# Kernel tuning notes

Hardware: AMD Instinct MI355X
Metric: run time of the kernel (lower is better)

The kernel has to match this reference:

```python
import jax, jax.numpy as jnp
import numpy as np

B, T, H, NH = 4, 4096, 768, 12
D = H          # attention inner dim (expand_ratio = 1)
I = 4 * H      # MLP intermediate size


def rms_norm(x, eps=1e-6):
    return x * jax.lax.rsqrt(jnp.mean(x * x, axis=-1, keepdims=True) + eps)


def layer_norm(x, eps=1e-6):
    mu = jnp.mean(x, axis=-1, keepdims=True)
    var = jnp.mean((x - mu) ** 2, axis=-1, keepdims=True)
    return (x - mu) * jax.lax.rsqrt(var + eps)


def act_quant(x):
    # per-token int8 absmax quantization (BitNet b1.58)
    scale = 127.0 / jnp.maximum(jnp.max(jnp.abs(x), axis=-1, keepdims=True), 1e-5)
    return jnp.clip(jnp.round(x * scale), -128, 127) / scale


def weight_quant(w):
    # per-tensor ternary quantization
    scale = 1.0 / jnp.maximum(jnp.mean(jnp.abs(w)), 1e-5)
    return jnp.clip(jnp.round(w * scale), -1, 1) / scale


def bit_linear(x, w, b=None):
    xn = rms_norm(x)
    xq = xn + jax.lax.stop_gradient(act_quant(xn) - xn)  # STE
    wq = w + jax.lax.stop_gradient(weight_quant(w) - w)  # STE
    y = jnp.einsum('...k,nk->...n', xq, wq)
    return y if b is None else y + b


def setup_inputs() -> dict:
    key = jax.random.key(0)
    ks = jax.random.split(key, 12)
    s = 0.02
    return dict(
        x=jax.random.normal(ks[0], (B, T, H), jnp.float32),
        c=jax.random.normal(ks[1], (B, H), jnp.float32),
        w_emb=jax.random.normal(ks[2], (2 * H, H), jnp.float32) * s,
        b_emb=jnp.zeros((2 * H,), jnp.float32),
        w_i=jax.random.normal(ks[3], (D, H), jnp.float32) * s,
        w_f=jax.random.normal(ks[4], (D, H), jnp.float32) * s,
        w_g=jax.random.normal(ks[5], (D, H), jnp.float32) * s,
        w_gn=jnp.ones((D,), jnp.float32),
        w_o=jax.random.normal(ks[6], (H, D), jnp.float32) * s,
        w_gate=jax.random.normal(ks[7], (2 * I, H), jnp.float32) * s,
        w_down=jax.random.normal(ks[8], (H, I), jnp.float32) * s,
        w_proj=jax.random.normal(ks[9], (H, 2 * H), jnp.float32) * s,
        b_proj=jnp.zeros((H,), jnp.float32),
    )


def reference(x, c, w_emb, b_emb, w_i, w_f, w_g, w_gn, w_o,
              w_gate, w_down, w_proj, b_proj):
    # --- AdaLayerNormZeroSingle ---
    emb = jnp.einsum('bk,nk->bn', jax.nn.silu(c), w_emb) + b_emb   # [B, 2H]
    scale, gate = jnp.split(emb, 2, axis=-1)                        # [B, H] each
    nx = layer_norm(x) * (1.0 + scale[:, None, :])                  # [B, T, H]

    # --- HGRNBitAttention: gated elementwise linear recurrence ---
    i = bit_linear(nx, w_i)                                         # [B, T, D]
    f = jax.nn.sigmoid(bit_linear(nx, w_f))                         # forget gate
    i = jax.nn.silu(i) * (1.0 - f)                                  # input gate

    def step(h, inp):
        it, ft = inp
        h = ft * h + it
        return h, h

    h0 = jnp.zeros((x.shape[0], i.shape[-1]), x.dtype)
    _, o = jax.lax.scan(step, h0, (jnp.swapaxes(i, 0, 1), jnp.swapaxes(f, 0, 1)))
    o = jnp.swapaxes(o, 0, 1)                                       # [B, T, D]

    g = bit_linear(nx, w_g)
    o = rms_norm(o) * w_gn * jax.nn.silu(g)                         # RMSNorm swish gate
    attn_out = bit_linear(o, w_o)                                   # [B, T, H]

    # --- HGRNBitMLP ---
    y = bit_linear(nx, w_gate)                                      # [B, T, 2I]
    g_m, y = jnp.split(y, 2, axis=-1)
    mlp_out = bit_linear(jax.nn.silu(g_m) * y, w_down)              # [B, T, H]

    # --- concat, project, gate, residual ---
    hs = jnp.concatenate([attn_out, mlp_out], axis=-1)              # [B, T, 2H]
    hs = gate[:, None, :] * bit_linear(hs, w_proj, b_proj)
    return x + hs
```

## Files before the change

kernel.cpp:

```cpp
#include <hip/hip_runtime.h>
#include <hip/hip_bf16.h>
#include <stdint.h>

#define HD 768
#define BB 4
#define TT 4096
#define NT (BB*TT)
#define IM 3072
#define NCH 128
#define CHL (TT/NCH)
#define MCH 4
#define MCT (NT/MCH)

typedef int v4i __attribute__((ext_vector_type(4)));
typedef __hip_bfloat16 bf16;
typedef unsigned int uint32;

__device__ __forceinline__ float wave_sum(float v){
#pragma unroll
  for (int o=32;o;o>>=1) v += __shfl_down(v,o);
  return v;
}
__device__ __forceinline__ float wave_sum_x(float v){
#pragma unroll
  for (int o=32;o;o>>=1) v += __shfl_xor(v,o);
  return v;
}
__device__ __forceinline__ float wave_max_x(float v){
#pragma unroll
  for (int o=32;o;o>>=1) v = fmaxf(v,__shfl_xor(v,o));
  return v;
}
__device__ __forceinline__ float block_sum(float v, float* lds){
  const int nw = blockDim.x >> 6;
  v = wave_sum(v);
  if ((threadIdx.x&63)==0) lds[threadIdx.x>>6] = v;
  __syncthreads();
  float r = lds[0];
  for (int i=1;i<nw;++i) r += lds[i];
  __syncthreads();
  return r;
}
__device__ __forceinline__ float sigmoidf_(float x){ return __builtin_amdgcn_rcpf(1.f + __expf(-x)); }
__device__ __forceinline__ float siluf_(float x){ return x * __builtin_amdgcn_rcpf(1.f + __expf(-x)); }
__device__ __forceinline__ float b2f(bf16 v){ return __bfloat162float(v); }
__device__ __forceinline__ bf16  f2b(float v){ return __float2bfloat16(v); }
__device__ __forceinline__ float bfb2f(uint32 u16){ uint32 v = u16<<16; return __builtin_bit_cast(float, v); }
__device__ __forceinline__ uint16_t packq2(float q0, float q1){
  int a = (int)q0, b = (int)q1;
  return (uint16_t)((a&0xff) | ((b&0xff)<<8));
}
__device__ __forceinline__ uint32 packq4(float a, float b, float c, float d){
  return (uint32)((int)a&0xff) | (((uint32)((int)b&0xff))<<8) |
         (((uint32)((int)c&0xff))<<16) | (((uint32)((int)d&0xff))<<24);
}
__device__ __forceinline__ uint32 pack2bf(float a, float b){
  uint32 ua = __builtin_bit_cast(uint16_t, f2b(a));
  uint32 ub = __builtin_bit_cast(uint16_t, f2b(b));
  return ua | (ub<<16);
}
__device__ __forceinline__ float clampq(float v){ return fminf(fmaxf(v,-128.f),127.f); }
__device__ __forceinline__ void gl_lds16(const int8_t* g, void* l){
  __builtin_amdgcn_global_load_lds((const __attribute__((address_space(1))) void*)g,
                                   (__attribute__((address_space(3))) void*)l, 16, 0, 0);
}

struct WArgs { const float* p[7]; int n[7]; size_t off[7]; };

#define WC1 589824
#define WC2 1179648
#define WC3 1769472
#define WC4 2359296
#define WC5 7077888
#define WC6 9437184
#define WCT 10616832

__global__ __launch_bounds__(256) void absum_part_all(WArgs wa, float* __restrict__ part){
  __shared__ float lds[8];
  const int seg = blockIdx.y;
  const int n4 = wa.n[seg] >> 2;
  const float4* w = (const float4*)wa.p[seg];
  float s = 0.f;
  for (int i = blockIdx.x*256 + threadIdx.x; i < n4; i += gridDim.x*256){
    float4 v = w[i];
    s += (fabsf(v.x)+fabsf(v.y)) + (fabsf(v.z)+fabsf(v.w));
  }
  s = block_sum(s, lds);
  if (threadIdx.x==0) part[seg*64 + blockIdx.x] = s;
}
__global__ __launch_bounds__(512) void absum_final_all(const float* __restrict__ part, WArgs wa,
                                                       float* __restrict__ wscv, float* __restrict__ wrec){
  int seg = threadIdx.x >> 6, lane = threadIdx.x & 63;
  float v = (seg < 7) ? part[seg*64 + lane] : 0.f;
  v = wave_sum(v);
  if (seg < 7 && lane == 0){
    float m = fmaxf(v / (float)wa.n[seg], 1e-5f);
    wscv[seg] = m; wrec[seg] = 1.f/m;
  }
}
__global__ __launch_bounds__(256) void wquant_all(WArgs wa, const float* __restrict__ wrec,
                                                  int8_t* __restrict__ q){
  const int seg = blockIdx.y;
  const int n4 = wa.n[seg] >> 2;
  const float4* p = (const float4*)wa.p[seg];
  uint32* qo = (uint32*)(q + wa.off[seg]);
  const float rc = wrec[seg];
  for (int i = blockIdx.x*256 + threadIdx.x; i < n4; i += gridDim.x*256){
    float4 v = p[i];
    int a  = (int)fminf(fmaxf(rintf(v.x*rc),-1.f),1.f);
    int b  = (int)fminf(fmaxf(rintf(v.y*rc),-1.f),1.f);
    int cc = (int)fminf(fmaxf(rintf(v.z*rc),-1.f),1.f);
    int d  = (int)fminf(fmaxf(rintf(v.w*rc),-1.f),1.f);
    qo[i] = (uint32)(a&0xff) | ((uint32)(b&0xff)<<8) | ((uint32)(cc&0xff)<<16) | ((uint32)(d&0xff)<<24);
  }
}

__global__ __launch_bounds__(256) void ada_emb(const float* __restrict__ c, const float* __restrict__ w_emb,
                                               const float* __restrict__ b_emb,
                                               float* __restrict__ scaleA, float* __restrict__ gateA){
  int o = blockIdx.x*4 + (threadIdx.x>>6);
  int lane = threadIdx.x & 63;
  int b = o / 1536, n = o % 1536;
  const float* cr = c + b*HD;
  const float* wr = w_emb + (size_t)n*HD;
  float s = 0.f;
  for (int k=lane; k<HD; k+=64){
    float cv = cr[k];
    s += siluf_(cv)*wr[k];
  }
  s = wave_sum(s);
  if (lane==0){
    s += b_emb[n];
    if (n < HD) scaleA[b*HD+n] = s;
    else        gateA[b*HD+(n-HD)] = s;
  }
}

__global__ __launch_bounds__(256) void ln_quant(const float* __restrict__ x, const float* __restrict__ scaleA,
                                                int8_t* __restrict__ xq, float* __restrict__ rsx){
  const int tok  = blockIdx.x*4 + (threadIdx.x>>6);
  const int lane = threadIdx.x & 63;
  const int b = tok >> 12;
  const float4* xr = (const float4*)(x + (size_t)tok*HD);
  const float4* sr = (const float4*)(scaleA + (size_t)b*HD);
  float4 v[3];
  float s1 = 0.f, s2 = 0.f;
#pragma unroll
  for (int j=0;j<3;++j){
    v[j] = xr[lane + j*64];
    s1 += (v[j].x+v[j].y)+(v[j].z+v[j].w);
    s2 += (v[j].x*v[j].x+v[j].y*v[j].y)+(v[j].z*v[j].z+v[j].w*v[j].w);
  }
  s1 = wave_sum_x(s1); s2 = wave_sum_x(s2);
  const float mu  = s1 * (1.f/768.f);
  const float var = fmaxf(s2 * (1.f/768.f) - mu*mu, 0.f);
  const float r1  = rsqrtf(var + 1e-6f);
  float sv[12]; float ms = 0.f, amr = 0.f;
#pragma unroll
  for (int j=0;j<3;++j){
    float4 sc = sr[lane + j*64];
    float a0 = (v[j].x-mu)*r1*(1.f+sc.x);
    float a1 = (v[j].y-mu)*r1*(1.f+sc.y);
    float a2 = (v[j].z-mu)*r1*(1.f+sc.z);
    float a3 = (v[j].w-mu)*r1*(1.f+sc.w);
    sv[4*j]=a0; sv[4*j+1]=a1; sv[4*j+2]=a2; sv[4*j+3]=a3;
    ms += (a0*a0+a1*a1)+(a2*a2+a3*a3);
    amr = fmaxf(amr, fmaxf(fmaxf(fabsf(a0),fabsf(a1)),fmaxf(fabsf(a2),fabsf(a3))));
  }
  ms = wave_sum_x(ms); amr = wave_max_x(amr);
  const float r2 = rsqrtf(ms*(1.f/768.f) + 1e-6f);
  const float am = fmaxf(amr*r2, 1e-5f);
  const float sx = 127.f/am;
  uint32* qo = (uint32*)(xq + (size_t)tok*HD);
#pragma unroll
  for (int j=0;j<3;++j){
    qo[lane + j*64] = packq4(clampq(rintf(sv[4*j]*r2*sx)),   clampq(rintf(sv[4*j+1]*r2*sx)),
                             clampq(rintf(sv[4*j+2]*r2*sx)), clampq(rintf(sv[4*j+3]*r2*sx)));
  }
  if (lane==0) rsx[tok] = am*(1.f/127.f);
}

template<int C>
__global__ __launch_bounds__(256) void rms_quant_w(const uint32* __restrict__ zin, int8_t* __restrict__ q,
                                                   float* __restrict__ rs){
  const int tok  = blockIdx.x*4 + (threadIdx.x>>6);
  const int lane = threadIdx.x & 63;
  const uint32* zp = zin + (size_t)tok*C*64;
  uint32 u[C]; float ss = 0.f, amr = 0.f;
#pragma unroll
  for (int j=0;j<C;++j){
    u[j] = zp[lane + j*64];
    float a = bfb2f(u[j] & 0xffff), b = bfb2f(u[j] >> 16);
    ss += a*a + b*b;
    amr = fmaxf(amr, fmaxf(fabsf(a),fabsf(b)));
  }
  ss = wave_sum_x(ss); amr = wave_max_x(amr);
  const float r = rsqrtf(ss*(1.f/(float)(C*128)) + 1e-6f);
  const float am = fmaxf(amr*r, 1e-5f);
  const float sx = 127.f/am;
  uint16_t* qo = (uint16_t*)(q + (size_t)tok*C*128);
#pragma unroll
  for (int j=0;j<C;++j){
    float a = bfb2f(u[j] & 0xffff), b = bfb2f(u[j] >> 16);
    qo[lane + j*64] = packq2(clampq(rintf(a*r*sx)), clampq(rintf(b*r*sx)));
  }
  if (lane==0) rs[tok] = am*(1.f/127.f);
}

__global__ __launch_bounds__(256) void rms_quant_cat(const uint32* __restrict__ pa, const uint32* __restrict__ pb,
                                                     int8_t* __restrict__ q, float* __restrict__ rs){
  const int tok  = blockIdx.x*4 + (threadIdx.x>>6);
  const int lane = threadIdx.x & 63;
  const uint32* ap = pa + (size_t)tok*(HD/2);
  const uint32* bp = pb + (size_t)tok*(HD/2);
  uint32 u[12]; float ss = 0.f, amr = 0.f;
#pragma unroll
  for (int j=0;j<6;++j){
    u[j] = ap[lane + j*64];
    float a = bfb2f(u[j] & 0xffff), b = bfb2f(u[j] >> 16);
    ss += a*a + b*b;
    amr = fmaxf(amr, fmaxf(fabsf(a),fabsf(b)));
  }
#pragma unroll
  for (int j=0;j<6;++j){
    u[6+j] = bp[lane + j*64];
    float a = bfb2f(u[6+j] & 0xffff), b = bfb2f(u[6+j] >> 16);
    ss += a*a + b*b;
    amr = fmaxf(amr, fmaxf(fabsf(a),fabsf(b)));
  }
  ss = wave_sum_x(ss); amr = wave_max_x(amr);
  const float r = rsqrtf(ss*(1.f/1536.f) + 1e-6f);
  const float am = fmaxf(amr*r, 1e-5f);
  const float sx = 127.f/am;
  uint16_t* qo = (uint16_t*)(q + (size_t)tok*(2*HD));
#pragma unroll
  for (int j=0;j<6;++j){
    float a = bfb2f(u[j] & 0xffff), b = bfb2f(u[j] >> 16);
    qo[lane + j*64] = packq2(clampq(rintf(a*r*sx)), clampq(rintf(b*r*sx)));
  }
#pragma unroll
  for (int j=0;j<6;++j){
    float a = bfb2f(u[6+j] & 0xffff), b = bfb2f(u[6+j] >> 16);
    qo[384 + lane + j*64] = packq2(clampq(rintf(a*r*sx)), clampq(rintf(b*r*sx)));
  }
  if (lane==0) rs[tok] = am*(1.f/127.f);
}

__global__ __launch_bounds__(256) void gate_norm_quant(const uint32* __restrict__ o, const uint32* __restrict__ gs,
                                                       const float* __restrict__ w_gn,
                                                       int8_t* __restrict__ oq, float* __restrict__ rso){
  const int tok  = blockIdx.x*4 + (threadIdx.x>>6);
  const int lane = threadIdx.x & 63;
  const uint32* op = o  + (size_t)tok*(HD/2);
  const uint32* gp = gs + (size_t)tok*(HD/2);
  const float2* wg = (const float2*)w_gn;
  uint32 u[6]; float ms = 0.f;
#pragma unroll
  for (int j=0;j<6;++j){
    u[j] = op[lane + j*64];
    float a = bfb2f(u[j] & 0xffff), b = bfb2f(u[j] >> 16);
    ms += a*a + b*b;
  }
  ms = wave_sum_x(ms);
  const float rn = rsqrtf(ms*(1.f/768.f) + 1e-6f);
  float uu[12]; float ms2 = 0.f, amr = 0.f;
#pragma unroll
  for (int j=0;j<6;++j){
    uint32 g = gp[lane + j*64];
    float2 w = wg[lane + j*64];
    float a = bfb2f(u[j] & 0xffff)*rn*w.x*bfb2f(g & 0xffff);
    float b = bfb2f(u[j] >> 16)  *rn*w.y*bfb2f(g >> 16);
    uu[2*j]=a; uu[2*j+1]=b;
    ms2 += a*a + b*b;
    amr = fmaxf(amr, fmaxf(fabsf(a),fabsf(b)));
  }
  ms2 = wave_sum_x(ms2); amr = wave_max_x(amr);
  const float r2 = rsqrtf(ms2*(1.f/768.f) + 1e-6f);
  const float am = fmaxf(amr*r2, 1e-5f);
  const float sx = 127.f/am;
  uint16_t* qo = (uint16_t*)(oq + (size_t)tok*HD);
#pragma unroll
  for (int j=0;j<6;++j){
    qo[lane + j*64] = packq2(clampq(rintf(uu[2*j]*r2*sx)), clampq(rintf(uu[2*j+1]*r2*sx)));
  }
  if (lane==0) rso[tok] = am*(1.f/127.f);
}

__global__ __launch_bounds__(384) void scan_pass1(const uint32* __restrict__ iact, const uint32* __restrict__ fsig,
                                                  float* __restrict__ chF, float* __restrict__ chH){
  const int blk = blockIdx.x;
  const int b = blk >> 7, ch = blk & (NCH-1);
  const int t0 = b*TT + ch*CHL;
  const size_t base = (size_t)t0*(HD/2) + threadIdx.x;
  float F0=1.f,F1=1.f,h0=0.f,h1=0.f;
#pragma unroll 4
  for (int s=0;s<CHL;++s){
    uint32 fu = fsig[base + (size_t)s*(HD/2)];
    uint32 iu = iact[base + (size_t)s*(HD/2)];
    float f0 = bfb2f(fu&0xffff), f1 = bfb2f(fu>>16);
    float a0 = bfb2f(iu&0xffff), a1 = bfb2f(iu>>16);
    h0 = f0*h0 + a0; h1 = f1*h1 + a1;
    F0 *= f0; F1 *= f1;
  }
  size_t cb = (size_t)blk*HD + 2*threadIdx.x;
  *(float2*)(chF + cb) = make_float2(F0,F1);
  *(float2*)(chH + cb) = make_float2(h0,h1);
}
__global__ __launch_bounds__(256) void scan_combine(float* __restrict__ chF, float* __restrict__ chH){
  const int gid = blockIdx.x*256 + threadIdx.x;
  const int b = gid / HD, d = gid % HD;
  float h = 0.f;
#pragma unroll 8
  for (int c=0;c<NCH;++c){
    size_t idx = (size_t)(b*NCH+c)*HD + d;
    float F = chF[idx], Hl = chH[idx];
    chH[idx] = h;
    h = F*h + Hl;
  }
}
__global__ __launch_bounds__(384) void scan_pass2(const uint32* iact, const uint32* __restrict__ fsig,
                                                  const float* __restrict__ chH, uint32* o){
  const int blk = blockIdx.x;
  const int b = blk >> 7, ch = blk & (NCH-1);
  const int t0 = b*TT + ch*CHL;
  const size_t base = (size_t)t0*(HD/2) + threadIdx.x;
  float2 hin = *(const float2*)(chH + (size_t)blk*HD + 2*threadIdx.x);
  float h0 = hin.x, h1 = hin.y;
#pragma unroll 4
  for (int s=0;s<CHL;++s){
    uint32 fu = fsig[base + (size_t)s*(HD/2)];
    uint32 iu = iact[base + (size_t)s*(HD/2)];
    float f0 = bfb2f(fu&0xffff), f1 = bfb2f(fu>>16);
    float a0 = bfb2f(iu&0xffff), a1 = bfb2f(iu>>16);
    h0 = f0*h0 + a0; h1 = f1*h1 + a1;
    uint16_t pa = __builtin_bit_cast(uint16_t, f2b(h0));
    uint16_t pb = __builtin_bit_cast(uint16_t, f2b(h1));
    o[base + (size_t)s*(HD/2)] = (uint32)pa | ((uint32)pb<<16);
  }
}

enum { EPI_IF=0, EPI_SILU=1, EPI_STORE=2, EPI_SWIGLU=3, EPI_PROJ=4 };

template<int EPI, bool DUAL>
__global__ __launch_bounds__(512) void gemm_i8(
    const int8_t* __restrict__ A, const float* __restrict__ rsA,
    const int8_t* __restrict__ B0, const int8_t* __restrict__ B1,
    const float* __restrict__ ws0p, const float* __restrict__ ws1p,
    int K, void* __restrict__ out0v, void* __restrict__ out1v,
    int ldOut, int colOff,
    const float* __restrict__ bias, const float* __restrict__ gateA,
    const float* __restrict__ xres)
{
  __shared__ __align__(16) uint8_t sA [2][16384];
  __shared__ __align__(16) uint8_t sB0[2][8192];
  __shared__ __align__(16) uint8_t sB1[DUAL?2:1][8192];

  const int lane = threadIdx.x & 63;
  const int wv   = threadIdx.x >> 6;
  const int m0 = blockIdx.x*256;
  const int n0 = blockIdx.y*128;
  const int wm = (wv>>1)*64;
  const int wn = (wv&1)*64;
  const int lr = lane & 15;
  const int sl = lane >> 4;

  const int8_t* gA[2]; const int8_t* gB0; const int8_t* gB1;
  int ldsOffA[2], ldsOffB;
#pragma unroll
  for (int j=0;j<2;++j){
    int q = wv*2 + j;
    int r = q*16 + (lane>>2);
    int cg = (lane&3) ^ ((r>>1)&3);
    gA[j] = A + (size_t)(m0+r)*K + cg*16;
    ldsOffA[j] = q*1024;
  }
  {
    int r = wv*16 + (lane>>2);
    int cg = (lane&3) ^ ((r>>1)&3);
    gB0 = B0 + (size_t)(n0+r)*K + cg*16;
    gB1 = DUAL ? (B1 + (size_t)(n0+r)*K + cg*16) : (const int8_t*)0;
    ldsOffB = wv*1024;
  }
  int offA[4], offB[4];
#pragma unroll
  for (int i=0;i<4;++i){
    int Ra = wm + i*16 + lr;
    offA[i] = Ra*64 + ((sl ^ ((Ra>>1)&3))<<4);
    int Rb = wn + i*16 + lr;
    offB[i] = Rb*64 + ((sl ^ ((Rb>>1)&3))<<4);
  }

  v4i acc0[4][4], acc1[4][4];
  const v4i vzero = {0,0,0,0};
#pragma unroll
  for (int i=0;i<4;++i)
#pragma unroll
    for (int j=0;j<4;++j){ acc0[i][j]=vzero; acc1[i][j]=vzero; }

  const int NTI = K >> 6;
#pragma unroll
  for (int j=0;j<2;++j) gl_lds16(gA[j], &sA[0][ldsOffA[j]]);
  gl_lds16(gB0, &sB0[0][ldsOffB]);
  if (DUAL) gl_lds16(gB1, &sB1[0][ldsOffB]);
#pragma unroll
  for (int j=0;j<2;++j) gl_lds16(gA[j]+64, &sA[1][ldsOffA[j]]);
  gl_lds16(gB0+64, &sB0[1][ldsOffB]);
  if (DUAL) gl_lds16(gB1+64, &sB1[1][ldsOffB]);

  int cur = 0;
  for (int t=0; t<NTI; ++t){
    if (t+1 < NTI){
      if constexpr (DUAL) asm volatile("s_waitcnt vmcnt(4)" ::: "memory");
      else                asm volatile("s_waitcnt vmcnt(3)" ::: "memory");
    } else {
      asm volatile("s_waitcnt vmcnt(0)" ::: "memory");
    }
    asm volatile("s_barrier" ::: "memory");

    v4i av[4], b0v[4], b1v[4];
#pragma unroll
    for (int i=0;i<4;++i){
      av[i]  = *(const v4i*)&sA [cur][offA[i]];
      b0v[i] = *(const v4i*)&sB0[cur][offB[i]];
    }
    if constexpr (DUAL){
#pragma unroll
      for (int i=0;i<4;++i) b1v[i] = *(const v4i*)&sB1[cur][offB[i]];
    }
    asm volatile("s_waitcnt lgkmcnt(0)" ::: "memory");
    asm volatile("s_barrier" ::: "memory");

    if (t+2 < NTI){
      const int ko = (t+2)*64;
#pragma unroll
      for (int j=0;j<2;++j) gl_lds16(gA[j]+ko, &sA[cur][ldsOffA[j]]);
      gl_lds16(gB0+ko, &sB0[cur][ldsOffB]);
      if (DUAL) gl_lds16(gB1+ko, &sB1[cur][ldsOffB]);
    }
    __builtin_amdgcn_sched_barrier(0);

    __builtin_amdgcn_s_setprio(1);
#pragma unroll
    for (int mi=0;mi<4;++mi){
#pragma unroll
      for (int ni=0;ni<4;++ni){
        acc0[mi][ni] = __builtin_amdgcn_mfma_i32_16x16x64_i8(b0v[ni], av[mi], acc0[mi][ni], 0,0,0);
        if constexpr (DUAL)
          acc1[mi][ni] = __builtin_amdgcn_mfma_i32_16x16x64_i8(b1v[ni], av[mi], acc1[mi][ni], 0,0,0);
      }
    }
    __builtin_amdgcn_s_setprio(0);
    cur ^= 1;
  }

  const float w0 = *ws0p;
  const float w1 = DUAL ? *ws1p : 0.f;
  const int rb = sl*4;
  const int em0 = m0 + wm, en0 = n0 + wn;
#pragma unroll
  for (int mi=0;mi<4;++mi){
    const int tok = em0 + mi*16 + lr;
    const float rs = rsA[tok];
#pragma unroll
    for (int ni=0;ni<4;++ni){
      const int ch = en0 + ni*16 + rb;
      float y0[4], y1[4];
#pragma unroll
      for (int r=0;r<4;++r){
        y0[r] = (float)acc0[mi][ni][r] * rs * w0;
        if constexpr (DUAL) y1[r] = (float)acc1[mi][ni][r] * rs * w1;
      }
      if constexpr (EPI==EPI_IF){
        float fs[4], io[4];
#pragma unroll
        for (int r=0;r<4;++r){ fs[r] = sigmoidf_(y1[r]); io[r] = siluf_(y0[r])*(1.f-fs[r]); }
        uint2 ui, uf;
        ui.x = pack2bf(io[0],io[1]); ui.y = pack2bf(io[2],io[3]);
        uf.x = pack2bf(fs[0],fs[1]); uf.y = pack2bf(fs[2],fs[3]);
        *(uint2*)((bf16*)out0v + (size_t)tok*ldOut + ch) = ui;
        *(uint2*)((bf16*)out1v + (size_t)tok*ldOut + ch) = uf;
      } else if constexpr (EPI==EPI_SILU){
        uint2 u;
        u.x = pack2bf(siluf_(y0[0]), siluf_(y0[1]));
        u.y = pack2bf(siluf_(y0[2]), siluf_(y0[3]));
        *(uint2*)((bf16*)out0v + (size_t)tok*ldOut + ch) = u;
      } else if constexpr (EPI==EPI_STORE){
        uint2 u;
        u.x = pack2bf(y0[0],y0[1]); u.y = pack2bf(y0[2],y0[3]);
        *(uint2*)((bf16*)out0v + (size_t)tok*ldOut + colOff + ch) = u;
      } else if constexpr (EPI==EPI_SWIGLU){
        uint2 u;
        u.x = pack2bf(siluf_(y0[0])*y1[0], siluf_(y0[1])*y1[1]);
        u.y = pack2bf(siluf_(y0[2])*y1[2], siluf_(y0[3])*y1[3]);
        *(uint2*)((bf16*)out0v + (size_t)tok*ldOut + ch) = u;
      } else {
        const int bidx = tok >> 12;
        float4 b4 = *(const float4*)(bias + ch);
        float4 g4 = *(const float4*)(gateA + bidx*HD + ch);
        float4 x4 = *(const float4*)(xres + (size_t)tok*HD + ch);
        float4 o4;
        o4.x = x4.x + g4.x*(y0[0] + b4.x);
        o4.y = x4.y + g4.y*(y0[1] + b4.y);
        o4.z = x4.z + g4.z*(y0[2] + b4.z);
        o4.w = x4.w + g4.w*(y0[3] + b4.w);
        *(float4*)((float*)out0v + (size_t)tok*HD + ch) = o4;
      }
    }
  }
}

extern "C" void kernel_launch(void* const* d_in, const int* in_sizes, int n_in,
                              void* d_out, int out_size, void* d_ws, size_t ws_size,
                              hipStream_t stream){
  const float* x      = (const float*)d_in[0];
  const float* c      = (const float*)d_in[1];
  const float* w_emb  = (const float*)d_in[2];
  const float* b_emb  = (const float*)d_in[3];
  const float* w_i    = (const float*)d_in[4];
  const float* w_f    = (const float*)d_in[5];
  const float* w_g    = (const float*)d_in[6];
  const float* w_gn   = (const float*)d_in[7];
  const float* w_o    = (const float*)d_in[8];
  const float* w_gate = (const float*)d_in[9];
  const float* w_down = (const float*)d_in[10];
  const float* w_proj = (const float*)d_in[11];
  const float* b_proj = (const float*)d_in[12];
  float* out = (float*)d_out;
  char* ws = (char*)d_ws;

  constexpr size_t SZ_HH   = (size_t)HD*HD;
  constexpr size_t o_wq     = 0;
  constexpr size_t o_wsc    = o_wq + (size_t)WCT;
  constexpr size_t o_wrecip = o_wsc    + 256;
  constexpr size_t o_part   = o_wrecip + 256;
  constexpr size_t o_scaleA = o_part   + 2048;
  constexpr size_t o_gateA  = o_scaleA + (size_t)BB*HD*4;
  constexpr size_t o_rsx    = o_gateA  + (size_t)BB*HD*4;
  constexpr size_t o_rso    = o_rsx    + (size_t)NT*4;
  constexpr size_t o_rsh    = o_rso    + (size_t)NT*4;
  constexpr size_t o_rsm    = o_rsh    + (size_t)NT*4;
  constexpr size_t o_xq     = o_rsm    + (size_t)NT*4;
  constexpr size_t o_END0   = o_xq     + (size_t)NT*HD;

  constexpr size_t o_R1     = o_END0;
  constexpr size_t o_R2     = o_R1     + (size_t)NT*HD*2;
  constexpr size_t o_R3     = o_R2     + (size_t)NT*HD*2;
  constexpr size_t o_chF    = o_R3     + (size_t)NT*HD*2;
  constexpr size_t o_chH    = o_chF    + (size_t)BB*NCH*HD*4;
  constexpr size_t o_R4     = o_chH    + (size_t)BB*NCH*HD*4;
  constexpr size_t NEED_S   = o_R4     + (size_t)NT*HD;

  constexpr size_t o_Z      = o_END0;
  constexpr size_t o_M      = o_Z + (size_t)NT*IM*2;
  constexpr size_t o_chF2   = o_M + (size_t)NT*IM;
  constexpr size_t o_chH2   = o_chF2 + (size_t)BB*NCH*HD*4;
  constexpr size_t NEED_B   = o_chH2 + (size_t)BB*NCH*HD*4;

  if (ws_size < NEED_S) return;
  const bool big = (ws_size >= NEED_B);

  float*  wscv  = (float*)(ws + o_wsc);
  float*  wrec  = (float*)(ws + o_wrecip);
  float*  part  = (float*)(ws + o_part);
  float*  scaleA= (float*)(ws + o_scaleA);
  float*  gateA = (float*)(ws + o_gateA);
  float*  rsx   = (float*)(ws + o_rsx);
  float*  rso   = (float*)(ws + o_rso);
  float*  rsh   = (float*)(ws + o_rsh);
  float*  rsm   = (float*)(ws + o_rsm);
  int8_t* xq    = (int8_t*)(ws + o_xq);
  int8_t* wqall = (int8_t*)(ws + o_wq);
  int8_t* wqp[7] = { wqall, wqall+WC1, wqall+WC2, wqall+WC3, wqall+WC4, wqall+WC5, wqall+WC6 };

  WArgs wa;
  wa.p[0]=w_i; wa.p[1]=w_f; wa.p[2]=w_g; wa.p[3]=w_o; wa.p[4]=w_gate; wa.p[5]=w_down; wa.p[6]=w_proj;
  wa.n[0]=(int)SZ_HH; wa.n[1]=(int)SZ_HH; wa.n[2]=(int)SZ_HH; wa.n[3]=(int)SZ_HH;
  wa.n[4]=2*IM*HD; wa.n[5]=HD*IM; wa.n[6]=HD*2*HD;
  wa.off[0]=0; wa.off[1]=WC1; wa.off[2]=WC2; wa.off[3]=WC3; wa.off[4]=WC4; wa.off[5]=WC5; wa.off[6]=WC6;

  absum_part_all <<<dim3(64,7),  dim3(256), 0, stream>>>(wa, part);
  absum_final_all<<<dim3(1),     dim3(512), 0, stream>>>(part, wa, wscv, wrec);
  wquant_all     <<<dim3(256,7), dim3(256), 0, stream>>>(wa, wrec, wqall);
  ada_emb <<<dim3(1536), dim3(256), 0, stream>>>(c, w_emb, b_emb, scaleA, gateA);
  ln_quant<<<dim3(NT/4), dim3(256), 0, stream>>>(x, scaleA, xq, rsx);

  if (big){
    bf16* zc      = (bf16*)(ws + o_Z);
    bf16* iact    = (bf16*)(ws + o_Z);
    bf16* fsig    = (bf16*)(ws + o_Z + (size_t)NT*HD*2);
    bf16* gsilu   = (bf16*)(ws + o_Z + (size_t)2*NT*HD*2);
    bf16* attn    = gsilu;
    bf16* mlp     = (bf16*)(ws + o_Z + (size_t)3*NT*HD*2);
    int8_t* mq    = (int8_t*)(ws + o_M);
    int8_t* oq    = (int8_t*)(ws + o_M);
    int8_t* hq    = (int8_t*)(ws + o_M + (size_t)NT*HD);
    float* chF    = (float*)(ws + o_chF2);
    float* chH    = (float*)(ws + o_chH2);
    bf16* obuf    = iact;

    gemm_i8<EPI_SWIGLU,true><<<dim3(NT/256,24), dim3(512), 0, stream>>>(
        xq, rsx, wqp[4], wqp[4] + (size_t)IM*HD, wscv+4, wscv+4, HD,
        zc, nullptr, IM, 0, nullptr, nullptr, nullptr);
    rms_quant_w<24><<<dim3(NT/4), dim3(256), 0, stream>>>((const uint32*)zc, mq, rsm);
    gemm_i8<EPI_STORE,false><<<dim3(NT/256,6), dim3(512), 0, stream>>>(
        mq, rsm, wqp[5], nullptr, wscv+5, nullptr, IM, mlp, nullptr, HD, 0, nullptr, nullptr, nullptr);

    gemm_i8<EPI_IF,true><<<dim3(NT/256,6), dim3(512), 0, stream>>>(
        xq, rsx, wqp[0], wqp[1], wscv+0, wscv+1, HD, iact, fsig, HD, 0, nullptr, nullptr, nullptr);
    gemm_i8<EPI_SILU,false><<<dim3(NT/256,6), dim3(512), 0, stream>>>(
        xq, rsx, wqp[2], nullptr, wscv+2, nullptr, HD, gsilu, nullptr, HD, 0, nullptr, nullptr, nullptr);
    scan_pass1 <<<dim3(BB*NCH), dim3(384), 0, stream>>>((const uint32*)iact, (const uint32*)fsig, chF, chH);
    scan_combine<<<dim3(12),    dim3(256), 0, stream>>>(chF, chH);
    scan_pass2 <<<dim3(BB*NCH), dim3(384), 0, stream>>>((const uint32*)iact, (const uint32*)fsig, chH, (uint32*)obuf);
    gate_norm_quant<<<dim3(NT/4), dim3(256), 0, stream>>>((const uint32*)obuf, (const uint32*)gsilu, w_gn, oq, rso);
    gemm_i8<EPI_STORE,false><<<dim3(NT/256,6), dim3(512), 0, stream>>>(
        oq, rso, wqp[3], nullptr, wscv+3, nullptr, HD, attn, nullptr, HD, 0, nullptr, nullptr, nullptr);

    rms_quant_cat<<<dim3(NT/4), dim3(256), 0, stream>>>((const uint32*)attn, (const uint32*)mlp, hq, rsh);
    gemm_i8<EPI_PROJ,false><<<dim3(NT/256,6), dim3(512), 0, stream>>>(
        hq, rsh, wqp[6], nullptr, wscv+6, nullptr, 2*HD, out, nullptr, HD, 0, b_proj, gateA, x);
  } else {
    bf16*   iact  = (bf16*)(ws + o_R1);
    bf16*   fsig  = (bf16*)(ws + o_R2);
    bf16*   gsilu = (bf16*)(ws + o_R3);
    bf16*   obuf  = iact;
    bf16*   hs    = (bf16*)(ws + o_R1);
    bf16*   zc    = (bf16*)(ws + o_R3);
    int8_t* hq    = (int8_t*)(ws + o_R3);
    float*  chF   = (float*)(ws + o_chF);
    float*  chH   = (float*)(ws + o_chH);
    int8_t* oq    = (int8_t*)(ws + o_R4);
    int8_t* mq    = (int8_t*)(ws + o_R4);

    gemm_i8<EPI_IF,true><<<dim3(NT/256,6), dim3(512), 0, stream>>>(
        xq, rsx, wqp[0], wqp[1], wscv+0, wscv+1, HD, iact, fsig, HD, 0, nullptr, nullptr, nullptr);
    gemm_i8<EPI_SILU,false><<<dim3(NT/256,6), dim3(512), 0, stream>>>(
        xq, rsx, wqp[2], nullptr, wscv+2, nullptr, HD, gsilu, nullptr, HD, 0, nullptr, nullptr, nullptr);
    scan_pass1 <<<dim3(BB*NCH), dim3(384), 0, stream>>>((const uint32*)iact, (const uint32*)fsig, chF, chH);
    scan_combine<<<dim3(12),    dim3(256), 0, stream>>>(chF, chH);
    scan_pass2 <<<dim3(BB*NCH), dim3(384), 0, stream>>>((const uint32*)iact, (const uint32*)fsig, chH, (uint32*)obuf);
    gate_norm_quant<<<dim3(NT/4), dim3(256), 0, stream>>>((const uint32*)obuf, (const uint32*)gsilu, w_gn, oq, rso);
    gemm_i8<EPI_STORE,false><<<dim3(NT/256,6), dim3(512), 0, stream>>>(
        oq, rso, wqp[3], nullptr, wscv+3, nullptr, HD, hs, nullptr, 2*HD, 0, nullptr, nullptr, nullptr);
    for (int cc=0; cc<MCH; ++cc){
      const size_t r0 = (size_t)cc*MCT;
      gemm_i8<EPI_SWIGLU,true><<<dim3(MCT/256,24), dim3(512), 0, stream>>>(
          xq + r0*HD, rsx + r0, wqp[4], wqp[4] + (size_t)IM*HD, wscv+4, wscv+4, HD,
          zc, nullptr, IM, 0, nullptr, nullptr, nullptr);
      rms_quant_w<24><<<dim3(MCT/4), dim3(256), 0, stream>>>((const uint32*)zc, mq, rsm);
      gemm_i8<EPI_STORE,false><<<dim3(MCT/256,6), dim3(512), 0, stream>>>(
          mq, rsm, wqp[5], nullptr, wscv+5, nullptr, IM,
          hs + r0*2*HD, nullptr, 2*HD, HD, nullptr, nullptr, nullptr);
    }
    rms_quant_w<12><<<dim3(NT/4), dim3(256), 0, stream>>>((const uint32*)hs, hq, rsh);
    gemm_i8<EPI_PROJ,false><<<dim3(NT/256,6), dim3(512), 0, stream>>>(
        hq, rsh, wqp[6], nullptr, wscv+6, nullptr, 2*HD, out, nullptr, HD, 0, b_proj, gateA, x);
  }

  (void)in_sizes; (void)n_in; (void)out_size;
}
```

Baseline: 445.7 us.

## Switch int8 GEMM to 32x32x32 MFMA with triple-buffered LDS pipeline

Replaces the 16x16x64 int8 MFMA tiling with 32x32x32 MFMA instructions, so each wave computes 2x2 tiles of 32x32 with 16-wide accumulators. This reduces LDS fragment reads per MFMA. The shared-memory ring grows from two to three stages, so the next tile's loads are issued before compute and only one barrier runs per iteration instead of two. LDS use rises (about 96KB for the dual variant), which may reduce occupancy. The epilogue is remapped to the 32x32 output layout.

New measurement: 504.1 us. 1.13x slower.

```diff
diff --git a/kernel.cpp b/kernel.cpp
--- a/kernel.cpp
+++ b/kernel.cpp
@@ -12,7 +12,8 @@
 #define MCH 4
 #define MCT (NT/MCH)
 
-typedef int v4i __attribute__((ext_vector_type(4)));
+typedef int v4i  __attribute__((ext_vector_type(4)));
+typedef int v16i __attribute__((ext_vector_type(16)));
 typedef __hip_bfloat16 bf16;
 typedef unsigned int uint32;
 
@@ -351,9 +352,9 @@
     const float* __restrict__ bias, const float* __restrict__ gateA,
     const float* __restrict__ xres)
 {
-  __shared__ __align__(16) uint8_t sA [2][16384];
-  __shared__ __align__(16) uint8_t sB0[2][8192];
-  __shared__ __align__(16) uint8_t sB1[DUAL?2:1][8192];
+  __shared__ __align__(16) uint8_t sA [3][16384];
+  __shared__ __align__(16) uint8_t sB0[3][8192];
+  __shared__ __align__(16) uint8_t sB1[DUAL?3:1][8192];
 
   const int lane = threadIdx.x & 63;
   const int wv   = threadIdx.x >> 6;
@@ -361,8 +362,8 @@
   const int n0 = blockIdx.y*128;
   const int wm = (wv>>1)*64;
   const int wn = (wv&1)*64;
-  const int lr = lane & 15;
-  const int sl = lane >> 4;
+  const int tokl = lane & 31;
+  const int hi   = lane >> 5;
 
   const int8_t* gA[2]; const int8_t* gB0; const int8_t* gB1;
   int ldsOffA[2], ldsOffB;
@@ -381,129 +382,156 @@
     gB1 = DUAL ? (B1 + (size_t)(n0+r)*K + cg*16) : (const int8_t*)0;
     ldsOffB = wv*1024;
   }
-  int offA[4], offB[4];
-#pragma unroll
-  for (int i=0;i<4;++i){
-    int Ra = wm + i*16 + lr;
-    offA[i] = Ra*64 + ((sl ^ ((Ra>>1)&3))<<4);
-    int Rb = wn + i*16 + lr;
-    offB[i] = Rb*64 + ((sl ^ ((Rb>>1)&3))<<4);
-  }
-
-  v4i acc0[4][4], acc1[4][4];
-  const v4i vzero = {0,0,0,0};
-#pragma unroll
-  for (int i=0;i<4;++i)
-#pragma unroll
-    for (int j=0;j<4;++j){ acc0[i][j]=vzero; acc1[i][j]=vzero; }
+  int offA[2][2], offB[2][2];
+#pragma unroll
+  for (int mi=0;mi<2;++mi)
+#pragma unroll
+    for (int ks=0;ks<2;++ks){
+      int Ra = wm + mi*32 + tokl;
+      offA[mi][ks] = Ra*64 + (((ks*2+hi) ^ ((Ra>>1)&3))<<4);
+    }
+#pragma unroll
+  for (int ni=0;ni<2;++ni)
+#pragma unroll
+    for (int ks=0;ks<2;++ks){
+      int Rb = wn + ni*32 + tokl;
+      offB[ni][ks] = Rb*64 + (((ks*2+hi) ^ ((Rb>>1)&3))<<4);
+    }
+
+  v16i acc0[2][2], acc1[2][2];
+  const v16i vzero = {0,0,0,0,0,0,0,0,0,0,0,0,0,0,0,0};
+#pragma unroll
+  for (int i=0;i<2;++i)
+#pragma unroll
+    for (int j=0;j<2;++j){ acc0[i][j]=vzero; acc1[i][j]=vzero; }
 
   const int NTI = K >> 6;
-#pragma unroll
-  for (int j=0;j<2;++j) gl_lds16(gA[j], &sA[0][ldsOffA[j]]);
-  gl_lds16(gB0, &sB0[0][ldsOffB]);
-  if (DUAL) gl_lds16(gB1, &sB1[0][ldsOffB]);
-#pragma unroll
-  for (int j=0;j<2;++j) gl_lds16(gA[j]+64, &sA[1][ldsOffA[j]]);
-  gl_lds16(gB0+64, &sB0[1][ldsOffB]);
-  if (DUAL) gl_lds16(gB1+64, &sB1[1][ldsOffB]);
-
-  int cur = 0;
+
+#define STAGE(KO, BUF) do { \
+    _Pragma("unroll") \
+    for (int j_=0;j_<2;++j_) gl_lds16(gA[j_]+(KO), &sA[BUF][ldsOffA[j_]]); \
+    gl_lds16(gB0+(KO), &sB0[BUF][ldsOffB]); \
+    if constexpr (DUAL) gl_lds16(gB1+(KO), &sB1[BUF][ldsOffB]); \
+  } while(0)
+
+#define WAIT_VM_LD() do { \
+    if constexpr (DUAL) asm volatile("s_waitcnt vmcnt(4)" ::: "memory"); \
+    else                asm volatile("s_waitcnt vmcnt(3)" ::: "memory"); \
+  } while(0)
+
+  STAGE(0, 0);
+  STAGE(64, 1);
+  WAIT_VM_LD();
+  asm volatile("s_barrier" ::: "memory");
+
+  int bc = 0, bn = 1, bs = 2;
   for (int t=0; t<NTI; ++t){
+    if (t+2 < NTI) STAGE((t+2)*64, bs);
+
+    v4i av[2][2], b0v[2][2], b1v[2][2];
+#pragma unroll
+    for (int mi=0;mi<2;++mi)
+#pragma unroll
+      for (int ks=0;ks<2;++ks)
+        av[mi][ks] = *(const v4i*)&sA[bc][offA[mi][ks]];
+#pragma unroll
+    for (int ni=0;ni<2;++ni)
+#pragma unroll
+      for (int ks=0;ks<2;++ks)
+        b0v[ni][ks] = *(const v4i*)&sB0[bc][offB[ni][ks]];
+    if constexpr (DUAL){
+#pragma unroll
+      for (int ni=0;ni<2;++ni)
+#pragma unroll
+        for (int ks=0;ks<2;++ks)
+          b1v[ni][ks] = *(const v4i*)&sB1[bc][offB[ni][ks]];
+    }
+
+    __builtin_amdgcn_s_setprio(1);
+#pragma unroll
+    for (int mi=0;mi<2;++mi)
+#pragma unroll
+      for (int ni=0;ni<2;++ni){
+        acc0[mi][ni] = __builtin_amdgcn_mfma_i32_32x32x32_i8(b0v[ni][0], av[mi][0], acc0[mi][ni], 0,0,0);
+        if constexpr (DUAL)
+          acc1[mi][ni] = __builtin_amdgcn_mfma_i32_32x32x32_i8(b1v[ni][0], av[mi][0], acc1[mi][ni], 0,0,0);
+      }
+#pragma unroll
+    for (int mi=0;mi<2;++mi)
+#pragma unroll
+      for (int ni=0;ni<2;++ni){
+        acc0[mi][ni] = __builtin_amdgcn_mfma_i32_32x32x32_i8(b0v[ni][1], av[mi][1], acc0[mi][ni], 0,0,0);
+        if constexpr (DUAL)
+          acc1[mi][ni] = __builtin_amdgcn_mfma_i32_32x32x32_i8(b1v[ni][1], av[mi][1], acc1[mi][ni], 0,0,0);
+      }
+    __builtin_amdgcn_s_setprio(0);
+
+    { int tmp = bc; bc = bn; bn = bs; bs = tmp; }
+
     if (t+1 < NTI){
-      if constexpr (DUAL) asm volatile("s_waitcnt vmcnt(4)" ::: "memory");
-      else                asm volatile("s_waitcnt vmcnt(3)" ::: "memory");
-    } else {
-      asm volatile("s_waitcnt vmcnt(0)" ::: "memory");
+      asm volatile("s_waitcnt lgkmcnt(0)" ::: "memory");
+      if (t+2 < NTI) WAIT_VM_LD();
+      else asm volatile("s_waitcnt vmcnt(0)" ::: "memory");
+      asm volatile("s_barrier" ::: "memory");
     }
-    asm volatile("s_barrier" ::: "memory");
-
-    v4i av[4], b0v[4], b1v[4];
-#pragma unroll
-    for (int i=0;i<4;++i){
-      av[i]  = *(const v4i*)&sA [cur][offA[i]];
-      b0v[i] = *(const v4i*)&sB0[cur][offB[i]];
-    }
-    if constexpr (DUAL){
-#pragma unroll
-      for (int i=0;i<4;++i) b1v[i] = *(const v4i*)&sB1[cur][offB[i]];
-    }
-    asm volatile("s_waitcnt lgkmcnt(0)" ::: "memory");
-    asm volatile("s_barrier" ::: "memory");
-
-    if (t+2 < NTI){
-      const int ko = (t+2)*64;
-#pragma unroll
-      for (int j=0;j<2;++j) gl_lds16(gA[j]+ko, &sA[cur][ldsOffA[j]]);
-      gl_lds16(gB0+ko, &sB0[cur][ldsOffB]);
-      if (DUAL) gl_lds16(gB1+ko, &sB1[cur][ldsOffB]);
-    }
-    __builtin_amdgcn_sched_barrier(0);
-
-    __builtin_amdgcn_s_setprio(1);
-#pragma unroll
-    for (int mi=0;mi<4;++mi){
-#pragma unroll
-      for (int ni=0;ni<4;++ni){
-        acc0[mi][ni] = __builtin_amdgcn_mfma_i32_16x16x64_i8(b0v[ni], av[mi], acc0[mi][ni], 0,0,0);
-        if constexpr (DUAL)
-          acc1[mi][ni] = __builtin_amdgcn_mfma_i32_16x16x64_i8(b1v[ni], av[mi], acc1[mi][ni], 0,0,0);
-      }
-    }
-    __builtin_amdgcn_s_setprio(0);
-    cur ^= 1;
-  }
+  }
+
+#undef STAGE
+#undef WAIT_VM_LD
 
   const float w0 = *ws0p;
   const float w1 = DUAL ? *ws1p : 0.f;
-  const int rb = sl*4;
   const int em0 = m0 + wm, en0 = n0 + wn;
 #pragma unroll
-  for (int mi=0;mi<4;++mi){
-    const int tok = em0 + mi*16 + lr;
+  for (int mi=0;mi<2;++mi){
+    const int tok = em0 + mi*32 + tokl;
     const float rs = rsA[tok];
 #pragma unroll
-    for (int ni=0;ni<4;++ni){
-      const int ch = en0 + ni*16 + rb;
-      float y0[4], y1[4];
-#pragma unroll
-      for (int r=0;r<4;++r){
-        y0[r] = (float)acc0[mi][ni][r] * rs * w0;
-        if constexpr (DUAL) y1[r] = (float)acc1[mi][ni][r] * rs * w1;
-      }
-      if constexpr (EPI==EPI_IF){
-        float fs[4], io[4];
-#pragma unroll
-        for (int r=0;r<4;++r){ fs[r] = sigmoidf_(y1[r]); io[r] = siluf_(y0[r])*(1.f-fs[r]); }
-        uint2 ui, uf;
-        ui.x = pack2bf(io[0],io[1]); ui.y = pack2bf(io[2],io[3]);
-        uf.x = pack2bf(fs[0],fs[1]); uf.y = pack2bf(fs[2],fs[3]);
-        *(uint2*)((bf16*)out0v + (size_t)tok*ldOut + ch) = ui;
-        *(uint2*)((bf16*)out1v + (size_t)tok*ldOut + ch) = uf;
-      } else if constexpr (EPI==EPI_SILU){
-        uint2 u;
-        u.x = pack2bf(siluf_(y0[0]), siluf_(y0[1]));
-        u.y = pack2bf(siluf_(y0[2]), siluf_(y0[3]));
-        *(uint2*)((bf16*)out0v + (size_t)tok*ldOut + ch) = u;
-      } else if constexpr (EPI==EPI_STORE){
-        uint2 u;
-        u.x = pack2bf(y0[0],y0[1]); u.y = pack2bf(y0[2],y0[3]);
-        *(uint2*)((bf16*)out0v + (size_t)tok*ldOut + colOff + ch) = u;
-      } else if constexpr (EPI==EPI_SWIGLU){
-        uint2 u;
-        u.x = pack2bf(siluf_(y0[0])*y1[0], siluf_(y0[1])*y1[1]);
-        u.y = pack2bf(siluf_(y0[2])*y1[2], siluf_(y0[3])*y1[3]);
-        *(uint2*)((bf16*)out0v + (size_t)tok*ldOut + ch) = u;
-      } else {
-        const int bidx = tok >> 12;
-        float4 b4 = *(const float4*)(bias + ch);
-        float4 g4 = *(const float4*)(gateA + bidx*HD + ch);
-        float4 x4 = *(const float4*)(xres + (size_t)tok*HD + ch);
-        float4 o4;
-        o4.x = x4.x + g4.x*(y0[0] + b4.x);
-        o4.y = x4.y + g4.y*(y0[1] + b4.y);
-        o4.z = x4.z + g4.z*(y0[2] + b4.z);
-        o4.w = x4.w + g4.w*(y0[3] + b4.w);
-        *(float4*)((float*)out0v + (size_t)tok*HD + ch) = o4;
+    for (int ni=0;ni<2;++ni){
+#pragma unroll
+      for (int q=0;q<4;++q){
+        const int ch = en0 + ni*32 + q*8 + hi*4;
+        float y0[4], y1[4];
+#pragma unroll
+        for (int r=0;r<4;++r){
+          y0[r] = (float)acc0[mi][ni][q*4+r] * rs * w0;
+          if constexpr (DUAL) y1[r] = (float)acc1[mi][ni][q*4+r] * rs * w1;
+        }
+        if constexpr (EPI==EPI_IF){
+          float fs[4], io[4];
+#pragma unroll
+          for (int r=0;r<4;++r){ fs[r] = sigmoidf_(y1[r]); io[r] = siluf_(y0[r])*(1.f-fs[r]); }
+          uint2 ui, uf;
+          ui.x = pack2bf(io[0],io[1]); ui.y = pack2bf(io[2],io[3]);
+          uf.x = pack2bf(fs[0],fs[1]); uf.y = pack2bf(fs[2],fs[3]);
+          *(uint2*)((bf16*)out0v + (size_t)tok*ldOut + ch) = ui;
+          *(uint2*)((bf16*)out1v + (size_t)tok*ldOut + ch) = uf;
+        } else if constexpr (EPI==EPI_SILU){
+          uint2 u;
+          u.x = pack2bf(siluf_(y0[0]), siluf_(y0[1]));
+          u.y = pack2bf(siluf_(y0[2]), siluf_(y0[3]));
+          *(uint2*)((bf16*)out0v + (size_t)tok*ldOut + ch) = u;
+        } else if constexpr (EPI==EPI_STORE){
+          uint2 u;
+          u.x = pack2bf(y0[0],y0[1]); u.y = pack2bf(y0[2],y0[3]);
+          *(uint2*)((bf16*)out0v + (size_t)tok*ldOut + colOff + ch) = u;
+        } else if constexpr (EPI==EPI_SWIGLU){
+          uint2 u;
+          u.x = pack2bf(siluf_(y0[0])*y1[0], siluf_(y0[1])*y1[1]);
+          u.y = pack2bf(siluf_(y0[2])*y1[2], siluf_(y0[3])*y1[3]);
+          *(uint2*)((bf16*)out0v + (size_t)tok*ldOut + ch) = u;
+        } else {
+          const int bidx = tok >> 12;
+          float4 b4 = *(const float4*)(bias + ch);
+          float4 g4 = *(const float4*)(gateA + bidx*HD + ch);
+          float4 x4 = *(const float4*)(xres + (size_t)tok*HD + ch);
+          float4 o4;
+          o4.x = x4.x + g4.x*(y0[0] + b4.x);
+          o4.y = x4.y + g4.y*(y0[1] + b4.y);
+          o4.z = x4.z + g4.z*(y0[2] + b4.z);
+          o4.w = x4.w + g4.w*(y0[3] + b4.w);
+          *(float4*)((float*)out0v + (size_t)tok*HD + ch) = o4;
+        }
       }
     }
   }
```

## Double int8 GEMM K-tile to 128 with 8-way LDS swizzle

Applied to the files above, without the earlier changes.

The int8 MFMA GEMM now stages 128-wide K slices instead of 64, doubling LDS buffers and using an 8-slot XOR swizzle. Each iteration runs two MFMA sub-steps over one barrier pair, halving the loop trip count and the barrier and wait overhead per unit of work. It also adds a launch-bounds occupancy hint of 2. LDS use rises to about 96KB for the dual variant, which may limit occupancy, and register pressure goes up from holding two fragment sets.

New measurement: 463.4 us. 1.04x slower.

```diff
diff --git a/kernel.cpp b/kernel.cpp
--- a/kernel.cpp
+++ b/kernel.cpp
@@ -342,7 +342,7 @@
 enum { EPI_IF=0, EPI_SILU=1, EPI_STORE=2, EPI_SWIGLU=3, EPI_PROJ=4 };
 
 template<int EPI, bool DUAL>
-__global__ __launch_bounds__(512) void gemm_i8(
+__global__ __launch_bounds__(512, 2) void gemm_i8(
     const int8_t* __restrict__ A, const float* __restrict__ rsA,
     const int8_t* __restrict__ B0, const int8_t* __restrict__ B1,
     const float* __restrict__ ws0p, const float* __restrict__ ws1p,
@@ -351,9 +351,9 @@
     const float* __restrict__ bias, const float* __restrict__ gateA,
     const float* __restrict__ xres)
 {
-  __shared__ __align__(16) uint8_t sA [2][16384];
-  __shared__ __align__(16) uint8_t sB0[2][8192];
-  __shared__ __align__(16) uint8_t sB1[DUAL?2:1][8192];
+  __shared__ __align__(16) uint8_t sA [2][32768];
+  __shared__ __align__(16) uint8_t sB0[2][16384];
+  __shared__ __align__(16) uint8_t sB1[DUAL?2:1][16384];
 
   const int lane = threadIdx.x & 63;
   const int wv   = threadIdx.x >> 6;
@@ -364,30 +364,34 @@
   const int lr = lane & 15;
   const int sl = lane >> 4;
 
-  const int8_t* gA[2]; const int8_t* gB0; const int8_t* gB1;
-  int ldsOffA[2], ldsOffB;
+  const int srow  = lane >> 3;
+  const int sslot = lane & 7;
+  const int8_t* gA[4]; int ldsOffA[4];
+#pragma unroll
+  for (int j=0;j<4;++j){
+    int q = wv*4 + j;
+    int r = q*8 + srow;
+    int cg = sslot ^ (r&7);
+    gA[j] = A + (size_t)(m0+r)*K + cg*16;
+    ldsOffA[j] = q*1024;
+  }
+  const int8_t* gB0[2]; const int8_t* gB1[2]; int ldsOffB[2];
 #pragma unroll
   for (int j=0;j<2;++j){
     int q = wv*2 + j;
-    int r = q*16 + (lane>>2);
-    int cg = (lane&3) ^ ((r>>1)&3);
-    gA[j] = A + (size_t)(m0+r)*K + cg*16;
-    ldsOffA[j] = q*1024;
-  }
-  {
-    int r = wv*16 + (lane>>2);
-    int cg = (lane&3) ^ ((r>>1)&3);
-    gB0 = B0 + (size_t)(n0+r)*K + cg*16;
-    gB1 = DUAL ? (B1 + (size_t)(n0+r)*K + cg*16) : (const int8_t*)0;
-    ldsOffB = wv*1024;
+    int r = q*8 + srow;
+    int cg = sslot ^ (r&7);
+    gB0[j] = B0 + (size_t)(n0+r)*K + cg*16;
+    gB1[j] = DUAL ? (B1 + (size_t)(n0+r)*K + cg*16) : (const int8_t*)0;
+    ldsOffB[j] = q*1024;
   }
   int offA[4], offB[4];
 #pragma unroll
   for (int i=0;i<4;++i){
     int Ra = wm + i*16 + lr;
-    offA[i] = Ra*64 + ((sl ^ ((Ra>>1)&3))<<4);
+    offA[i] = Ra*128 + ((sl ^ (Ra&7))<<4);
     int Rb = wn + i*16 + lr;
-    offB[i] = Rb*64 + ((sl ^ ((Rb>>1)&3))<<4);
+    offB[i] = Rb*128 + ((sl ^ (Rb&7))<<4);
   }
 
   v4i acc0[4][4], acc1[4][4];
@@ -397,61 +401,87 @@
 #pragma unroll
     for (int j=0;j<4;++j){ acc0[i][j]=vzero; acc1[i][j]=vzero; }
 
-  const int NTI = K >> 6;
-#pragma unroll
-  for (int j=0;j<2;++j) gl_lds16(gA[j], &sA[0][ldsOffA[j]]);
-  gl_lds16(gB0, &sB0[0][ldsOffB]);
-  if (DUAL) gl_lds16(gB1, &sB1[0][ldsOffB]);
-#pragma unroll
-  for (int j=0;j<2;++j) gl_lds16(gA[j]+64, &sA[1][ldsOffA[j]]);
-  gl_lds16(gB0+64, &sB0[1][ldsOffB]);
-  if (DUAL) gl_lds16(gB1+64, &sB1[1][ldsOffB]);
+  const int NTI = K >> 7;
+
+#define STAGE(KO, BUF) do { \
+    _Pragma("unroll") \
+    for (int j_=0;j_<4;++j_) gl_lds16(gA[j_]+(KO), &sA[BUF][ldsOffA[j_]]); \
+    _Pragma("unroll") \
+    for (int j_=0;j_<2;++j_){ \
+      gl_lds16(gB0[j_]+(KO), &sB0[BUF][ldsOffB[j_]]); \
+      if constexpr (DUAL) gl_lds16(gB1[j_]+(KO), &sB1[BUF][ldsOffB[j_]]); \
+    } \
+  } while(0)
+
+#define WAIT_VM_LD() do { \
+    if constexpr (DUAL) asm volatile("s_waitcnt vmcnt(8)" ::: "memory"); \
+    else                asm volatile("s_waitcnt vmcnt(6)" ::: "memory"); \
+  } while(0)
+
+#define MMA(AV, B0V, B1V) do { \
+    __builtin_amdgcn_s_setprio(1); \
+    _Pragma("unroll") \
+    for (int mi_=0;mi_<4;++mi_){ \
+      _Pragma("unroll") \
+      for (int ni_=0;ni_<4;++ni_){ \
+        acc0[mi_][ni_] = __builtin_amdgcn_mfma_i32_16x16x64_i8(B0V[ni_], AV[mi_], acc0[mi_][ni_], 0,0,0); \
+        if constexpr (DUAL) \
+          acc1[mi_][ni_] = __builtin_amdgcn_mfma_i32_16x16x64_i8(B1V[ni_], AV[mi_], acc1[mi_][ni_], 0,0,0); \
+      } \
+    } \
+    __builtin_amdgcn_s_setprio(0); \
+  } while(0)
+
+  STAGE(0, 0);
+  STAGE(128, 1);
 
   int cur = 0;
   for (int t=0; t<NTI; ++t){
     if (t+1 < NTI){
-      if constexpr (DUAL) asm volatile("s_waitcnt vmcnt(4)" ::: "memory");
-      else                asm volatile("s_waitcnt vmcnt(3)" ::: "memory");
+      WAIT_VM_LD();
     } else {
       asm volatile("s_waitcnt vmcnt(0)" ::: "memory");
     }
     asm volatile("s_barrier" ::: "memory");
 
-    v4i av[4], b0v[4], b1v[4];
-#pragma unroll
-    for (int i=0;i<4;++i){
-      av[i]  = *(const v4i*)&sA [cur][offA[i]];
-      b0v[i] = *(const v4i*)&sB0[cur][offB[i]];
+    {
+      v4i av[4], b0v[4], b1v[4];
+#pragma unroll
+      for (int i=0;i<4;++i){
+        av[i]  = *(const v4i*)&sA [cur][offA[i]];
+        b0v[i] = *(const v4i*)&sB0[cur][offB[i]];
+      }
+      if constexpr (DUAL){
+#pragma unroll
+        for (int i=0;i<4;++i) b1v[i] = *(const v4i*)&sB1[cur][offB[i]];
+      }
+      MMA(av, b0v, b1v);
     }
-    if constexpr (DUAL){
-#pragma unroll
-      for (int i=0;i<4;++i) b1v[i] = *(const v4i*)&sB1[cur][offB[i]];
+    {
+      v4i av[4], b0v[4], b1v[4];
+#pragma unroll
+      for (int i=0;i<4;++i){
+        av[i]  = *(const v4i*)&sA [cur][offA[i]^64];
+        b0v[i] = *(const v4i*)&sB0[cur][offB[i]^64];
+      }
+      if constexpr (DUAL){
+#pragma unroll
+        for (int i=0;i<4;++i) b1v[i] = *(const v4i*)&sB1[cur][offB[i]^64];
+      }
+      asm volatile("s_waitcnt lgkmcnt(0)" ::: "memory");
+      asm volatile("s_barrier" ::: "memory");
+      if (t+2 < NTI){
+        STAGE((t+2)*128, cur);
+      }
+      __builtin_amdgcn_sched_barrier(0);
+      MMA(av, b0v, b1v);
     }
-    asm volatile("s_waitcnt lgkmcnt(0)" ::: "memory");
-    asm volatile("s_barrier" ::: "memory");
-
-    if (t+2 < NTI){
-      const int ko = (t+2)*64;
-#pragma unroll
-      for (int j=0;j<2;++j) gl_lds16(gA[j]+ko, &sA[cur][ldsOffA[j]]);
-      gl_lds16(gB0+ko, &sB0[cur][ldsOffB]);
-      if (DUAL) gl_lds16(gB1+ko, &sB1[cur][ldsOffB]);
-    }
-    __builtin_amdgcn_sched_barrier(0);
-
-    __builtin_amdgcn_s_setprio(1);
-#pragma unroll
-    for (int mi=0;mi<4;++mi){
-#pragma unroll
-      for (int ni=0;ni<4;++ni){
-        acc0[mi][ni] = __builtin_amdgcn_mfma_i32_16x16x64_i8(b0v[ni], av[mi], acc0[mi][ni], 0,0,0);
-        if constexpr (DUAL)
-          acc1[mi][ni] = __builtin_amdgcn_mfma_i32_16x16x64_i8(b1v[ni], av[mi], acc1[mi][ni], 0,0,0);
-      }
-    }
-    __builtin_amdgcn_s_setprio(0);
     cur ^= 1;
   }
+
+#undef STAGE
+#undef WAIT_VM_LD
+#undef MMA
 
   const float w0 = *ws0p;
   const float w1 = DUAL ? *ws1p : 0.f;
```
